# Optimization experiments

Hardware: AMD Instinct MI355X
Metric: run time of the kernel (lower is better)

Reference implementation:

```python
import jax, jax.numpy as jnp
import numpy as np


def setup_inputs() -> dict:
    key = jax.random.key(0)
    k1, k2, k3 = jax.random.split(key, 3)
    B, H, S, D = 4, 16, 2048, 64
    return {
        "key": jax.random.normal(k1, (B, H, S, D), dtype=jnp.float32),
        "value": jax.random.normal(k2, (B, H, S, D), dtype=jnp.float32),
        "query": jax.random.normal(k3, (B, H, S, D), dtype=jnp.float32),
        # causal mask: True = attend, matches torch masked_fill_(~mask, -inf)
        "mask": jnp.tril(jnp.ones((S, S), dtype=jnp.bool_)),
    }


def reference(key, value, query, mask):
    # scores[b,h,q,k] = query . key^T  (mask applied before scaling as in the
    # source; -inf survives the divide so this equals standard masked attn)
    d = key.shape[-1]
    scores = jnp.einsum("bhqd,bhkd->bhqk", query, key)
    scores = jnp.where(mask, scores, -jnp.inf)
    scores = scores / jnp.sqrt(jnp.asarray(d, dtype=scores.dtype))
    attn = jax.nn.softmax(scores, axis=-1)
    # dropout omitted for a deterministic reference (eval mode)
    return jnp.einsum("bhqk,bhkd->bhqd", attn, value)
```

## Files before the change

kernel.cpp:

```cpp
#include <hip/hip_runtime.h>
#include <hip/hip_bf16.h>

typedef __attribute__((ext_vector_type(4))) float  f32x4;
typedef __attribute__((ext_vector_type(16))) float f32x16;
typedef __attribute__((ext_vector_type(8))) short  bf16x8v;
typedef __attribute__((ext_vector_type(4))) short  bf16x4v;

__device__ __forceinline__ unsigned short f2bf(float x) {
  union { float f; unsigned u; } v; v.f = x;
  unsigned r = v.u + 0x7FFF + ((v.u >> 16) & 1);
  return (unsigned short)(r >> 16);
}
__device__ __forceinline__ unsigned pk2(float lo, float hi2) {
  return (unsigned)f2bf(lo) | ((unsigned)f2bf(hi2) << 16);
}

constexpr int S  = 2048;
constexpr int D  = 64;
constexpr int BQ = 128;
constexpr int BK = 64;

__global__ __launch_bounds__(256, 3) void attn_fwd(
    const float* __restrict__ Kg, const float* __restrict__ Vg,
    const float* __restrict__ Qg, float* __restrict__ Og) {
  __shared__ unsigned short Kl[BK * D];
  __shared__ unsigned short Vt[D * BK];

  const int tid  = threadIdx.x;
  const int lane = tid & 63;
  const int w    = tid >> 6;
  const int l31  = lane & 31;
  const int hi   = lane >> 5;

  const int qb = 15 - (int)(blockIdx.x & 15);
  const int bh = blockIdx.x >> 4;
  const int q0 = qb * BQ;

  const size_t base = (size_t)bh * S * D;
  const float* Kp = Kg + base;
  const float* Vp = Vg + base;
  const float* Qp = Qg + base;
  float*       Op = Og + base;

  const int qrow = q0 + w * 32 + l31;

  bf16x8v qf[4];
#pragma unroll
  for (int c = 0; c < 4; ++c) {
    const float* src = Qp + (size_t)qrow * D + c * 16 + hi * 8;
    f32x4 a = *(const f32x4*)src;
    f32x4 b = *(const f32x4*)(src + 4);
    bf16x8v f;
    f[0] = f2bf(a[0]); f[1] = f2bf(a[1]); f[2] = f2bf(a[2]); f[3] = f2bf(a[3]);
    f[4] = f2bf(b[0]); f[5] = f2bf(b[1]); f[6] = f2bf(b[2]); f[7] = f2bf(b[3]);
    qf[c] = f;
  }

  f32x16 acc0, acc1;
#pragma unroll
  for (int i = 0; i < 16; ++i) { acc0[i] = 0.f; acc1[i] = 0.f; }
  float mr = -INFINITY, lsum = 0.f;

  const int ktmax      = (q0 + BQ - 1) >> 6;
  const int wave_ktmax = (q0 + 32 * w + 31) >> 6;

  for (int kt = 0; kt <= ktmax; ++kt) {
    __syncthreads();
    {
      const int row = tid >> 2;
      const int cq  = tid & 3;
      const float* ks = Kp + (size_t)(kt * BK + row) * D;
#pragma unroll
      for (int i = 0; i < 4; ++i) {
        const int col = (cq + 4 * i) * 4;
        f32x4 kv = *(const f32x4*)(ks + col);
        bf16x4v kb;
        kb[0] = f2bf(kv[0]); kb[1] = f2bf(kv[1]);
        kb[2] = f2bf(kv[2]); kb[3] = f2bf(kv[3]);
        *(bf16x4v*)((char*)Kl + row * 128 + ((col * 2) ^ ((row & 7) << 4))) = kb;
      }
    }
    {
      const int kgrp = tid >> 4;
      const int dgrp = tid & 15;
      const int k0 = kgrp * 4, d0 = dgrp * 4;
      const float* vs = Vp + (size_t)(kt * BK + k0) * D + d0;
      f32x4 r0 = *(const f32x4*)(vs);
      f32x4 r1 = *(const f32x4*)(vs + D);
      f32x4 r2 = *(const f32x4*)(vs + 2 * D);
      f32x4 r3 = *(const f32x4*)(vs + 3 * D);
#pragma unroll
      for (int j = 0; j < 4; ++j) {
        const int d = d0 + j;
        bf16x4v tb;
        tb[0] = f2bf(r0[j]); tb[1] = f2bf(r1[j]);
        tb[2] = f2bf(r2[j]); tb[3] = f2bf(r3[j]);
        *(bf16x4v*)((char*)Vt + d * 128 + ((k0 * 2) ^ ((d & 7) << 4))) = tb;
      }
    }
    __syncthreads();

    if (kt <= wave_ktmax) {
      const int swz = (l31 & 7) << 4;

      f32x16 s0, s1;
#pragma unroll
      for (int i = 0; i < 16; ++i) { s0[i] = 0.f; s1[i] = 0.f; }
#pragma unroll
      for (int c = 0; c < 4; ++c) {
        const int kb = c * 32 + hi * 16;
        bf16x8v ka0 = *(const bf16x8v*)((char*)Kl + l31 * 128 + (kb ^ swz));
        s0 = __builtin_amdgcn_mfma_f32_32x32x16_bf16(ka0, qf[c], s0, 0, 0, 0);
        bf16x8v ka1 = *(const bf16x8v*)((char*)Kl + (32 + l31) * 128 + (kb ^ swz));
        s1 = __builtin_amdgcn_mfma_f32_32x32x16_bf16(ka1, qf[c], s1, 0, 0, 0);
      }

#pragma unroll
      for (int r = 0; r < 16; ++r) {
        const int crow = (r & 3) + 8 * (r >> 2) + 4 * hi;
        const int key0 = kt * BK + crow;
        s0[r] = (key0      <= qrow) ? s0[r] * 0.125f : -INFINITY;
        s1[r] = (key0 + 32 <= qrow) ? s1[r] * 0.125f : -INFINITY;
      }

      float t[16];
#pragma unroll
      for (int r = 0; r < 16; ++r) t[r] = fmaxf(s0[r], s1[r]);
#pragma unroll
      for (int st = 8; st >= 1; st >>= 1)
#pragma unroll
        for (int i = 0; i < 8; ++i)
          if (i < st) t[i] = fmaxf(t[i], t[i + st]);
      float mx = fmaxf(t[0], __shfl_xor(t[0], 32));
      const float mnew = fmaxf(mr, mx);
      const float corr = __expf(mr - mnew);
      mr = mnew;

#pragma unroll
      for (int r = 0; r < 16; ++r) {
        s0[r] = __expf(s0[r] - mnew);
        s1[r] = __expf(s1[r] - mnew);
      }
      float u[16];
#pragma unroll
      for (int r = 0; r < 16; ++r) u[r] = s0[r] + s1[r];
#pragma unroll
      for (int st = 8; st >= 1; st >>= 1)
#pragma unroll
        for (int i = 0; i < 8; ++i)
          if (i < st) u[i] = u[i] + u[i + st];
      float ps = u[0] + __shfl_xor(u[0], 32);
      lsum = lsum * corr + ps;
#pragma unroll
      for (int i = 0; i < 16; ++i) { acc0[i] *= corr; acc1[i] *= corr; }

#pragma unroll
      for (int c = 0; c < 4; ++c) {
        const int rb = (c & 1) * 8;
        float p0, p1, p2, p3, p4, p5, p6, p7;
        if (c & 2) {
          p0 = s1[rb+0]; p1 = s1[rb+1]; p2 = s1[rb+2]; p3 = s1[rb+3];
          p4 = s1[rb+4]; p5 = s1[rb+5]; p6 = s1[rb+6]; p7 = s1[rb+7];
        } else {
          p0 = s0[rb+0]; p1 = s0[rb+1]; p2 = s0[rb+2]; p3 = s0[rb+3];
          p4 = s0[rb+4]; p5 = s0[rb+5]; p6 = s0[rb+6]; p7 = s0[rb+7];
        }
        const unsigned a0 = pk2(p0, p1), a1 = pk2(p2, p3);
        const unsigned b0 = pk2(p4, p5), b1 = pk2(p6, p7);
        const unsigned oa0 = (unsigned)__shfl_xor((int)a0, 32);
        const unsigned oa1 = (unsigned)__shfl_xor((int)a1, 32);
        const unsigned ob0 = (unsigned)__shfl_xor((int)b0, 32);
        const unsigned ob1 = (unsigned)__shfl_xor((int)b1, 32);
        union { unsigned u4[4]; bf16x8v v; } pw;
        pw.u4[0] = hi ? ob0 : a0;
        pw.u4[1] = hi ? ob1 : a1;
        pw.u4[2] = hi ? b0  : oa0;
        pw.u4[3] = hi ? b1  : oa1;
        const int kb = c * 32 + hi * 16;
        bf16x8v v0 = *(const bf16x8v*)((char*)Vt + l31 * 128 + (kb ^ swz));
        acc0 = __builtin_amdgcn_mfma_f32_32x32x16_bf16(v0, pw.v, acc0, 0, 0, 0);
        bf16x8v v1 = *(const bf16x8v*)((char*)Vt + (32 + l31) * 128 + (kb ^ swz));
        acc1 = __builtin_amdgcn_mfma_f32_32x32x16_bf16(v1, pw.v, acc1, 0, 0, 0);
      }
    }
  }

  const float inv = 1.0f / lsum;
#pragma unroll
  for (int mq = 0; mq < 4; ++mq) {
    const int dbase = 8 * mq + 4 * hi;
    f32x4 o0, o1;
#pragma unroll
    for (int i = 0; i < 4; ++i) {
      o0[i] = acc0[4 * mq + i] * inv;
      o1[i] = acc1[4 * mq + i] * inv;
    }
    *(f32x4*)(Op + (size_t)qrow * D + dbase)      = o0;
    *(f32x4*)(Op + (size_t)qrow * D + 32 + dbase) = o1;
  }
}

extern "C" void kernel_launch(void* const* d_in, const int* in_sizes, int n_in,
                              void* d_out, int out_size, void* d_ws, size_t ws_size,
                              hipStream_t stream) {
  const float* Kg = (const float*)d_in[0];
  const float* Vg = (const float*)d_in[1];
  const float* Qg = (const float*)d_in[2];
  float* Og = (float*)d_out;

  const int BH = 4 * 16;
  dim3 grid(BH * (S / BQ));
  dim3 block(256);
  attn_fwd<<<grid, block, 0, stream>>>(Kg, Vg, Qg, Og);
}
```

Measured before the change: 291.8 us.

## Double query tile to 256 rows, prefetch K/V tiles, use exp2 softmax

Raises the query block to 256 rows with 512-thread blocks, so each K/V tile staged in LDS serves eight waves instead of four. The global loads of the next K/V tile are issued into registers before the compute of the current one, overlapping memory latency with MFMA work, and K and V staging is split between the two halves of the block. The causal mask is applied only on the diagonal tile, and the softmax uses exp2 with the scale folded into an FMA and flatter max/sum reductions. In exchange the grid has half as many blocks and each thread holds more registers for the prefetch, which may lower occupancy.

```diff
diff --git a/kernel.cpp b/kernel.cpp
--- a/kernel.cpp
+++ b/kernel.cpp
@@ -7,9 +7,8 @@
 typedef __attribute__((ext_vector_type(4))) short  bf16x4v;
 
 __device__ __forceinline__ unsigned short f2bf(float x) {
-  union { float f; unsigned u; } v; v.f = x;
-  unsigned r = v.u + 0x7FFF + ((v.u >> 16) & 1);
-  return (unsigned short)(r >> 16);
+  __bf16 h = (__bf16)x;
+  return __builtin_bit_cast(unsigned short, h);
 }
 __device__ __forceinline__ unsigned pk2(float lo, float hi2) {
   return (unsigned)f2bf(lo) | ((unsigned)f2bf(hi2) << 16);
@@ -17,10 +16,11 @@
 
 constexpr int S  = 2048;
 constexpr int D  = 64;
-constexpr int BQ = 128;
+constexpr int BQ = 256;
 constexpr int BK = 64;
-
-__global__ __launch_bounds__(256, 3) void attn_fwd(
+#define KSCALE 0.18033688011112042f
+
+__global__ __launch_bounds__(512, 4) void attn_fwd(
     const float* __restrict__ Kg, const float* __restrict__ Vg,
     const float* __restrict__ Qg, float* __restrict__ Og) {
   __shared__ unsigned short Kl[BK * D];
@@ -32,8 +32,8 @@
   const int l31  = lane & 31;
   const int hi   = lane >> 5;
 
-  const int qb = 15 - (int)(blockIdx.x & 15);
-  const int bh = blockIdx.x >> 4;
+  const int qb = 7 - (int)(blockIdx.x & 7);
+  const int bh = blockIdx.x >> 3;
   const int q0 = qb * BQ;
 
   const size_t base = (size_t)bh * S * D;
@@ -43,6 +43,46 @@
   float*       Op = Og + base;
 
   const int qrow = q0 + w * 32 + l31;
+
+  const int  st  = tid & 255;
+  const bool isK = tid < 256;
+  const int  krow = st >> 2, kcol0 = 16 * (st & 3);
+  const int  kby0 = kcol0 * 2, kswz = (krow & 7) << 4;
+  const int  vk0 = 4 * (st >> 4), vd0 = 4 * (st & 15);
+
+  f32x4 pf0, pf1, pf2, pf3;
+
+  auto LOAD = [&](int kt) {
+    if (isK) {
+      const float* p = Kp + (size_t)(kt * BK + krow) * D + kcol0;
+      pf0 = *(const f32x4*)(p);      pf1 = *(const f32x4*)(p + 4);
+      pf2 = *(const f32x4*)(p + 8);  pf3 = *(const f32x4*)(p + 12);
+    } else {
+      const float* p = Vp + (size_t)(kt * BK + vk0) * D + vd0;
+      pf0 = *(const f32x4*)(p);          pf1 = *(const f32x4*)(p + D);
+      pf2 = *(const f32x4*)(p + 2 * D);  pf3 = *(const f32x4*)(p + 3 * D);
+    }
+  };
+  auto WRITE = [&]() {
+    if (isK) {
+      bf16x8v c0, c1;
+      c0[0] = f2bf(pf0[0]); c0[1] = f2bf(pf0[1]); c0[2] = f2bf(pf0[2]); c0[3] = f2bf(pf0[3]);
+      c0[4] = f2bf(pf1[0]); c0[5] = f2bf(pf1[1]); c0[6] = f2bf(pf1[2]); c0[7] = f2bf(pf1[3]);
+      c1[0] = f2bf(pf2[0]); c1[1] = f2bf(pf2[1]); c1[2] = f2bf(pf2[2]); c1[3] = f2bf(pf2[3]);
+      c1[4] = f2bf(pf3[0]); c1[5] = f2bf(pf3[1]); c1[6] = f2bf(pf3[2]); c1[7] = f2bf(pf3[3]);
+      *(bf16x8v*)((char*)Kl + krow * 128 + ((kby0)      ^ kswz)) = c0;
+      *(bf16x8v*)((char*)Kl + krow * 128 + ((kby0 + 16) ^ kswz)) = c1;
+    } else {
+#pragma unroll
+      for (int j = 0; j < 4; ++j) {
+        const int d = vd0 + j;
+        bf16x4v tb;
+        tb[0] = f2bf(pf0[j]); tb[1] = f2bf(pf1[j]);
+        tb[2] = f2bf(pf2[j]); tb[3] = f2bf(pf3[j]);
+        *(bf16x4v*)((char*)Vt + d * 128 + ((vk0 * 2) ^ ((d & 7) << 4))) = tb;
+      }
+    }
+  };
 
   bf16x8v qf[4];
 #pragma unroll
@@ -61,46 +101,18 @@
   for (int i = 0; i < 16; ++i) { acc0[i] = 0.f; acc1[i] = 0.f; }
   float mr = -INFINITY, lsum = 0.f;
 
-  const int ktmax      = (q0 + BQ - 1) >> 6;
-  const int wave_ktmax = (q0 + 32 * w + 31) >> 6;
+  const int ktmax   = 4 * qb + 3;
+  const int wave_dt = (q0 + 32 * w) >> 6;
+
+  LOAD(0);
 
   for (int kt = 0; kt <= ktmax; ++kt) {
     __syncthreads();
-    {
-      const int row = tid >> 2;
-      const int cq  = tid & 3;
-      const float* ks = Kp + (size_t)(kt * BK + row) * D;
-#pragma unroll
-      for (int i = 0; i < 4; ++i) {
-        const int col = (cq + 4 * i) * 4;
-        f32x4 kv = *(const f32x4*)(ks + col);
-        bf16x4v kb;
-        kb[0] = f2bf(kv[0]); kb[1] = f2bf(kv[1]);
-        kb[2] = f2bf(kv[2]); kb[3] = f2bf(kv[3]);
-        *(bf16x4v*)((char*)Kl + row * 128 + ((col * 2) ^ ((row & 7) << 4))) = kb;
-      }
-    }
-    {
-      const int kgrp = tid >> 4;
-      const int dgrp = tid & 15;
-      const int k0 = kgrp * 4, d0 = dgrp * 4;
-      const float* vs = Vp + (size_t)(kt * BK + k0) * D + d0;
-      f32x4 r0 = *(const f32x4*)(vs);
-      f32x4 r1 = *(const f32x4*)(vs + D);
-      f32x4 r2 = *(const f32x4*)(vs + 2 * D);
-      f32x4 r3 = *(const f32x4*)(vs + 3 * D);
-#pragma unroll
-      for (int j = 0; j < 4; ++j) {
-        const int d = d0 + j;
-        bf16x4v tb;
-        tb[0] = f2bf(r0[j]); tb[1] = f2bf(r1[j]);
-        tb[2] = f2bf(r2[j]); tb[3] = f2bf(r3[j]);
-        *(bf16x4v*)((char*)Vt + d * 128 + ((k0 * 2) ^ ((d & 7) << 4))) = tb;
-      }
-    }
+    WRITE();
+    if (kt < ktmax) LOAD(kt + 1);
     __syncthreads();
 
-    if (kt <= wave_ktmax) {
+    if (kt <= wave_dt) {
       const int swz = (l31 & 7) << 4;
 
       f32x16 s0, s1;
@@ -115,41 +127,47 @@
         s1 = __builtin_amdgcn_mfma_f32_32x32x16_bf16(ka1, qf[c], s1, 0, 0, 0);
       }
 
+      if (kt == wave_dt) {
+#pragma unroll
+        for (int r = 0; r < 16; ++r) {
+          const int crow = (r & 3) + 8 * (r >> 2) + 4 * hi;
+          const int key0 = kt * BK + crow;
+          if (key0      > qrow) s0[r] = -INFINITY;
+          if (key0 + 32 > qrow) s1[r] = -INFINITY;
+        }
+      }
+
+      float a0 = fmaxf(s0[0], s1[0]), a1 = fmaxf(s0[1], s1[1]);
+      float a2 = fmaxf(s0[2], s1[2]), a3 = fmaxf(s0[3], s1[3]);
+#pragma unroll
+      for (int r = 4; r < 16; r += 4) {
+        a0 = fmaxf(a0, fmaxf(s0[r],     s1[r]));
+        a1 = fmaxf(a1, fmaxf(s0[r + 1], s1[r + 1]));
+        a2 = fmaxf(a2, fmaxf(s0[r + 2], s1[r + 2]));
+        a3 = fmaxf(a3, fmaxf(s0[r + 3], s1[r + 3]));
+      }
+      float mx = fmaxf(fmaxf(a0, a1), fmaxf(a2, a3));
+      mx = fmaxf(mx, __shfl_xor(mx, 32));
+      const float mnew = fmaxf(mr, mx);
+      const float corr = __builtin_amdgcn_exp2f((mr - mnew) * KSCALE);
+      mr = mnew;
+      const float nb = mnew * KSCALE;
 #pragma unroll
       for (int r = 0; r < 16; ++r) {
-        const int crow = (r & 3) + 8 * (r >> 2) + 4 * hi;
-        const int key0 = kt * BK + crow;
-        s0[r] = (key0      <= qrow) ? s0[r] * 0.125f : -INFINITY;
-        s1[r] = (key0 + 32 <= qrow) ? s1[r] * 0.125f : -INFINITY;
-      }
-
-      float t[16];
-#pragma unroll
-      for (int r = 0; r < 16; ++r) t[r] = fmaxf(s0[r], s1[r]);
-#pragma unroll
-      for (int st = 8; st >= 1; st >>= 1)
-#pragma unroll
-        for (int i = 0; i < 8; ++i)
-          if (i < st) t[i] = fmaxf(t[i], t[i + st]);
-      float mx = fmaxf(t[0], __shfl_xor(t[0], 32));
-      const float mnew = fmaxf(mr, mx);
-      const float corr = __expf(mr - mnew);
-      mr = mnew;
-
-#pragma unroll
-      for (int r = 0; r < 16; ++r) {
-        s0[r] = __expf(s0[r] - mnew);
-        s1[r] = __expf(s1[r] - mnew);
-      }
-      float u[16];
-#pragma unroll
-      for (int r = 0; r < 16; ++r) u[r] = s0[r] + s1[r];
-#pragma unroll
-      for (int st = 8; st >= 1; st >>= 1)
-#pragma unroll
-        for (int i = 0; i < 8; ++i)
-          if (i < st) u[i] = u[i] + u[i + st];
-      float ps = u[0] + __shfl_xor(u[0], 32);
+        s0[r] = __builtin_amdgcn_exp2f(__builtin_fmaf(s0[r], KSCALE, -nb));
+        s1[r] = __builtin_amdgcn_exp2f(__builtin_fmaf(s1[r], KSCALE, -nb));
+      }
+      float u0 = s0[0] + s1[0], u1 = s0[1] + s1[1];
+      float u2 = s0[2] + s1[2], u3 = s0[3] + s1[3];
+#pragma unroll
+      for (int r = 4; r < 16; r += 4) {
+        u0 += s0[r]     + s1[r];
+        u1 += s0[r + 1] + s1[r + 1];
+        u2 += s0[r + 2] + s1[r + 2];
+        u3 += s0[r + 3] + s1[r + 3];
+      }
+      float ps = (u0 + u1) + (u2 + u3);
+      ps += __shfl_xor(ps, 32);
       lsum = lsum * corr + ps;
 #pragma unroll
       for (int i = 0; i < 16; ++i) { acc0[i] *= corr; acc1[i] *= corr; }
@@ -165,17 +183,17 @@
           p0 = s0[rb+0]; p1 = s0[rb+1]; p2 = s0[rb+2]; p3 = s0[rb+3];
           p4 = s0[rb+4]; p5 = s0[rb+5]; p6 = s0[rb+6]; p7 = s0[rb+7];
         }
-        const unsigned a0 = pk2(p0, p1), a1 = pk2(p2, p3);
-        const unsigned b0 = pk2(p4, p5), b1 = pk2(p6, p7);
-        const unsigned oa0 = (unsigned)__shfl_xor((int)a0, 32);
-        const unsigned oa1 = (unsigned)__shfl_xor((int)a1, 32);
-        const unsigned ob0 = (unsigned)__shfl_xor((int)b0, 32);
-        const unsigned ob1 = (unsigned)__shfl_xor((int)b1, 32);
+        const unsigned a0u = pk2(p0, p1), a1u = pk2(p2, p3);
+        const unsigned b0u = pk2(p4, p5), b1u = pk2(p6, p7);
+        const unsigned oa0 = (unsigned)__shfl_xor((int)a0u, 32);
+        const unsigned oa1 = (unsigned)__shfl_xor((int)a1u, 32);
+        const unsigned ob0 = (unsigned)__shfl_xor((int)b0u, 32);
+        const unsigned ob1 = (unsigned)__shfl_xor((int)b1u, 32);
         union { unsigned u4[4]; bf16x8v v; } pw;
-        pw.u4[0] = hi ? ob0 : a0;
-        pw.u4[1] = hi ? ob1 : a1;
-        pw.u4[2] = hi ? b0  : oa0;
-        pw.u4[3] = hi ? b1  : oa1;
+        pw.u4[0] = hi ? ob0 : a0u;
+        pw.u4[1] = hi ? ob1 : a1u;
+        pw.u4[2] = hi ? b0u : oa0;
+        pw.u4[3] = hi ? b1u : oa1;
         const int kb = c * 32 + hi * 16;
         bf16x8v v0 = *(const bf16x8v*)((char*)Vt + l31 * 128 + (kb ^ swz));
         acc0 = __builtin_amdgcn_mfma_f32_32x32x16_bf16(v0, pw.v, acc0, 0, 0, 0);
@@ -210,6 +228,6 @@
 
   const int BH = 4 * 16;
   dim3 grid(BH * (S / BQ));
-  dim3 block(256);
+  dim3 block(512);
   attn_fwd<<<grid, block, 0, stream>>>(Kg, Vg, Qg, Og);
 }
```

Measured after the change: 255.7 us. -12.3%, faster.
